# Kernel optimization log

Measured on AMD Instinct MI355X. Metric: run time of the kernel, lower is better.

Reference implementation:

```python
import jax, jax.numpy as jnp
import numpy as np

I_DECAY = 0.95
STAG_THRESH = 0.95
MAX_GATE = 0.6
MIN_I_GATE = 0.25
EPS = 1e-12


def setup_inputs() -> dict:
    key = jax.random.key(0)
    ks = jax.random.split(key, 9)
    B, T, D_IN, D_OUT = 4, 2048, 2048, 2048
    x = jax.random.normal(ks[0], (B, T, D_IN), dtype=jnp.float32)
    s = 1.0 / np.sqrt(D_IN)
    Wp = jax.random.uniform(ks[1], (D_IN, D_OUT), jnp.float32, -s, s)
    Wi = jax.random.uniform(ks[2], (D_IN, D_OUT), jnp.float32, -s, s) * 0.3
    Wd = jax.random.uniform(ks[3], (D_IN, D_OUT), jnp.float32, -s, s) * 0.3
    gate_w = jax.random.uniform(ks[4], (D_IN, 3), jnp.float32, -s, s)
    gate_b = jnp.array([0.5, 0.0, 0.0], dtype=jnp.float32)
    kick_vec = jax.random.normal(ks[5], (D_OUT,), dtype=jnp.float32) * 0.01
    kick_w = jax.random.uniform(ks[6], (D_IN, 1), jnp.float32, -s, s)
    kick_b = jnp.full((1,), -2.0, dtype=jnp.float32)
    bias = jnp.zeros((D_OUT,), dtype=jnp.float32)
    return {"x": x, "Wp": Wp, "Wi": Wi, "Wd": Wd, "gate_w": gate_w,
            "gate_b": gate_b, "kick_vec": kick_vec, "kick_w": kick_w,
            "kick_b": kick_b, "bias": bias}


def _ema_integral(x, decay):
    # x: [B,T,D] -> time-major scan; integral[0] = x[0]
    xt = jnp.swapaxes(x, 0, 1)  # [T,B,D]

    def step(carry, xcur):
        new = decay * carry + (1.0 - decay) * xcur
        return new, new

    init = xt[0]
    _, rest = jax.lax.scan(step, init, xt[1:])
    integral = jnp.concatenate([init[None], rest], axis=0)
    return jnp.swapaxes(integral, 0, 1)  # [B,T,D]


def reference(x, Wp, Wi, Wd, gate_w, gate_b, kick_vec, kick_w, kick_b, bias):
    B, T, D = x.shape
    # --- EMA integral (linear recurrence over T) ---
    integral = _ema_integral(x, I_DECAY)

    # --- stagnation-aware derivative ---
    diff = jnp.concatenate(
        [jnp.zeros_like(x[:, :1]), x[:, 1:] - x[:, :-1]], axis=1)
    x_norm = x / jnp.maximum(
        jnp.linalg.norm(x, axis=-1, keepdims=True), EPS)
    cos_sim = jnp.concatenate(
        [jnp.zeros((B, 1), x.dtype),
         jnp.sum(x_norm[:, 1:] * x_norm[:, :-1], axis=-1)], axis=1)  # [B,T]
    stagnation = (cos_sim > STAG_THRESH).astype(x.dtype)
    kick_strength = jax.nn.sigmoid(
        jnp.einsum('btd,do->bto', x, kick_w) + kick_b)[..., 0]  # [B,T]
    derivative = diff + (stagnation * kick_strength)[..., None] * kick_vec

    # --- gates: softmax -> clamp max -> clamp I min -> renormalize ---
    g = jax.nn.softmax(jnp.einsum('btd,dg->btg', x, gate_w) + gate_b, axis=-1)
    g = jnp.minimum(g, MAX_GATE)
    g = g.at[..., 1].set(jnp.maximum(g[..., 1], MIN_I_GATE))
    g = g / jnp.sum(g, axis=-1, keepdims=True)

    out = (g[..., 0:1] * jnp.einsum('btd,do->bto', x, Wp)
           + g[..., 1:2] * jnp.einsum('btd,do->bto', integral, Wi)
           + g[..., 2:3] * jnp.einsum('btd,do->bto', derivative, Wd))
    return out + bias
```

## Files before the change

### kernel.cpp

```cpp
#include <hip/hip_runtime.h>

#define DH 2048
#define TT 2048
#define BB 4
#define MROWS 8192
#define NZ 6144
#define NCH 128
#define LCH 16
#define LAM 0.44012667f
#define LAM2 1.982646e-06f

typedef __attribute__((ext_vector_type(8))) short bf16x8;
typedef __attribute__((ext_vector_type(4))) float f32x4;

__device__ __forceinline__ unsigned short f2bf(float f) {
  union { float f; unsigned int u; } v; v.f = f;
  unsigned int u = v.u;
  return (unsigned short)((u + 0x7FFFu + ((u >> 16) & 1u)) >> 16);
}
__device__ __forceinline__ float bf2f(unsigned short u) {
  union { unsigned int i; float f; } v; v.i = ((unsigned int)u) << 16;
  return v.f;
}
__device__ __forceinline__ void gld16(const unsigned short* g, unsigned short* l) {
  __builtin_amdgcn_global_load_lds((const __attribute__((address_space(1))) void*)g,
                                   (__attribute__((address_space(3))) void*)l, 16, 0, 0);
}

__global__ __launch_bounds__(256) void prep_w(const float* __restrict__ Wp,
                                              const float* __restrict__ Wi,
                                              const float* __restrict__ Wd,
                                              const float* __restrict__ kick_vec,
                                              unsigned short* __restrict__ Wt,
                                              float* __restrict__ kvWd) {
  __shared__ float tile[64][65];
  int bid = blockIdx.x;
  int mat = bid >> 10;
  int t2 = bid & 1023;
  int dt = (t2 >> 5) * 64;
  int ot = (t2 & 31) * 64;
  const float* W = (mat == 0) ? Wp : ((mat == 1) ? Wi : Wd);
  int nbase = mat * DH;
  int tid = threadIdx.x;
  int r = tid >> 4;
  int c4 = (tid & 15) * 4;
#pragma unroll
  for (int i = 0; i < 4; ++i) {
    int rr = r + i * 16;
    float4 v = *(const float4*)&W[(size_t)(dt + rr) * DH + ot + c4];
    tile[rr][c4 + 0] = v.x; tile[rr][c4 + 1] = v.y;
    tile[rr][c4 + 2] = v.z; tile[rr][c4 + 3] = v.w;
  }
  __syncthreads();
  int o = tid >> 3;
  int d8 = (tid & 7) * 8;
#pragma unroll
  for (int pass = 0; pass < 2; ++pass) {
    int oo = o + pass * 32;
    union { unsigned short u[8]; uint4 v; } pk;
#pragma unroll
    for (int i = 0; i < 8; ++i) pk.u[i] = f2bf(tile[d8 + i][oo]);
    *(uint4*)&Wt[(size_t)(nbase + ot + oo) * DH + dt + d8] = pk.v;
  }
  if (mat == 2 && tid < 64) {
    float s = 0.f;
#pragma unroll 8
    for (int dd = 0; dd < 64; ++dd) s += kick_vec[dt + dd] * tile[dd][tid];
    atomicAdd(&kvWd[ot + tid], s);
  }
}

__global__ __launch_bounds__(256) void conv_x(const float* __restrict__ x,
                                              const float* __restrict__ gate_w,
                                              const float* __restrict__ gate_b,
                                              const float* __restrict__ kick_w,
                                              const float* __restrict__ kick_b,
                                              float* __restrict__ rs,
                                              unsigned short* __restrict__ A) {
  int r = blockIdx.x;
  int t = r & (TT - 1);
  const float* xr = x + (size_t)r * DH;
  const float* xq = xr - DH;
  const bool hp = (t != 0);
  int tid = threadIdx.x;
  float a0 = 0, a1 = 0, a2 = 0, ak = 0, axx = 0, apx = 0, app = 0;
#pragma unroll
  for (int it = 0; it < 2; ++it) {
    int d0 = (tid + it * 256) * 4;
    float4 xv = *(const float4*)(xr + d0);
    float4 pv = hp ? *(const float4*)(xq + d0) : make_float4(0.f, 0.f, 0.f, 0.f);
    float4 q0 = *(const float4*)(gate_w + (size_t)d0 * 3);
    float4 q1 = *(const float4*)(gate_w + (size_t)d0 * 3 + 4);
    float4 q2 = *(const float4*)(gate_w + (size_t)d0 * 3 + 8);
    float4 kw = *(const float4*)(kick_w + d0);
    float xa[4] = {xv.x, xv.y, xv.z, xv.w};
    float pa[4] = {pv.x, pv.y, pv.z, pv.w};
    a0 += xa[0] * q0.x + xa[1] * q0.w + xa[2] * q1.z + xa[3] * q2.y;
    a1 += xa[0] * q0.y + xa[1] * q1.x + xa[2] * q1.w + xa[3] * q2.z;
    a2 += xa[0] * q0.z + xa[1] * q1.y + xa[2] * q2.x + xa[3] * q2.w;
    ak += xa[0] * kw.x + xa[1] * kw.y + xa[2] * kw.z + xa[3] * kw.w;
    union { unsigned short u[4]; uint2 v; } pk;
#pragma unroll
    for (int j = 0; j < 4; ++j) {
      axx += xa[j] * xa[j];
      apx += xa[j] * pa[j];
      app += pa[j] * pa[j];
      pk.u[j] = f2bf(xa[j]);
    }
    *(uint2*)&A[(size_t)r * DH + d0] = pk.v;
  }
#pragma unroll
  for (int off = 32; off > 0; off >>= 1) {
    a0 += __shfl_xor(a0, off); a1 += __shfl_xor(a1, off);
    a2 += __shfl_xor(a2, off); ak += __shfl_xor(ak, off);
    axx += __shfl_xor(axx, off); apx += __shfl_xor(apx, off);
    app += __shfl_xor(app, off);
  }
  __shared__ float red[4][7];
  int wv = tid >> 6;
  if ((tid & 63) == 0) {
    red[wv][0] = a0; red[wv][1] = a1; red[wv][2] = a2; red[wv][3] = ak;
    red[wv][4] = axx; red[wv][5] = apx; red[wv][6] = app;
  }
  __syncthreads();
  if (tid == 0) {
    float v[7];
#pragma unroll
    for (int i = 0; i < 7; ++i) v[i] = red[0][i] + red[1][i] + red[2][i] + red[3][i];
    float l0 = v[0] + gate_b[0], l1 = v[1] + gate_b[1], l2 = v[2] + gate_b[2];
    float mx = fmaxf(l0, fmaxf(l1, l2));
    float e0 = expf(l0 - mx), e1 = expf(l1 - mx), e2 = expf(l2 - mx);
    float inv = 1.f / (e0 + e1 + e2);
    float G0 = fminf(e0 * inv, 0.6f);
    float G1 = fminf(e1 * inv, 0.6f);
    float G2 = fminf(e2 * inv, 0.6f);
    G1 = fmaxf(G1, 0.25f);
    float inv2 = 1.f / (G0 + G1 + G2);
    G0 *= inv2; G1 *= inv2; G2 *= inv2;
    float ks = 1.f / (1.f + expf(-(v[3] + kick_b[0])));
    float nn = fmaxf(sqrtf(v[4]), 1e-12f) * fmaxf(sqrtf(v[6]), 1e-12f);
    float cs = hp ? (v[5] / nn) : 0.f;
    float cc = (cs > 0.95f) ? (G2 * ks) : 0.f;
    *(float4*)(rs + (size_t)r * 4) = make_float4(G0, G1, G2, cc);
  }
}


#define BAR __builtin_amdgcn_s_barrier()
#define VMW8 asm volatile("s_waitcnt vmcnt(8)" ::: "memory")
#define VMW4 asm volatile("s_waitcnt vmcnt(4)" ::: "memory")
#define VMW2 asm volatile("s_waitcnt vmcnt(2)" ::: "memory")
#define VMW0 asm volatile("s_waitcnt vmcnt(0)" ::: "memory")
#define LGK0 asm volatile("s_waitcnt lgkmcnt(0)" ::: "memory")

#define ST_A(bf, h, kt) do { \
  gld16(pA + (size_t)((h) * 64) * DH + (kt) * 64,       lA + (bf) * 16384 + (h) * 8192 + ldsW); \
  gld16(pA + (size_t)((h) * 64 + 128) * DH + (kt) * 64, lA + (bf) * 16384 + (h) * 8192 + 4096 + ldsW); \
} while (0)
#define ST_B(bf, g, kt) do { \
  gld16(pB + (size_t)((g) * 32) * DH + (kt) * 64,       lB + (bf) * 16384 + (g) * 8192 + ldsW); \
  gld16(pB + (size_t)((g) * 32 + 128) * DH + (kt) * 64, lB + (bf) * 16384 + (g) * 8192 + 4096 + ldsW); \
} while (0)

#define RD_A(bf, h) do { \
  const unsigned short* p_ = lA + (bf) * 16384 + (h) * 8192 + aRd; \
  _Pragma("unroll") \
  for (int mi_ = 0; mi_ < 4; ++mi_) { \
    av[mi_][0] = *(const bf16x8*)(p_ + mi_ * 1024 + kph0); \
    av[mi_][1] = *(const bf16x8*)(p_ + mi_ * 1024 + kph1); \
  } \
} while (0)
#define RD_B(bf, g) do { \
  const unsigned short* p_ = lB + (bf) * 16384 + (g) * 8192 + bRd; \
  _Pragma("unroll") \
  for (int ni_ = 0; ni_ < 2; ++ni_) { \
    bv[g][ni_][0] = *(const bf16x8*)(p_ + ni_ * 1024 + kph0); \
    bv[g][ni_][1] = *(const bf16x8*)(p_ + ni_ * 1024 + kph1); \
  } \
} while (0)

#define MM(h, g) do { \
  __builtin_amdgcn_s_setprio(1); \
  _Pragma("unroll") \
  for (int mi_ = 0; mi_ < 4; ++mi_) { \
    _Pragma("unroll") \
    for (int ni_ = 0; ni_ < 2; ++ni_) { \
      f32x4 c_ = acc[(h) * 4 + mi_][(g) * 2 + ni_]; \
      c_ = __builtin_amdgcn_mfma_f32_16x16x32_bf16(av[mi_][0], bv[g][ni_][0], c_, 0, 0, 0); \
      c_ = __builtin_amdgcn_mfma_f32_16x16x32_bf16(av[mi_][1], bv[g][ni_][1], c_, 0, 0, 0); \
      acc[(h) * 4 + mi_][(g) * 2 + ni_] = c_; \
    } \
  } \
  __builtin_amdgcn_s_setprio(0); \
} while (0)

__global__ __launch_bounds__(512, 2) void gemm_kernel(const unsigned short* __restrict__ A,
                                                      const unsigned short* __restrict__ Bt,
                                                      unsigned short* __restrict__ Z,
                                                      unsigned short* __restrict__ cpb) {
  __shared__ __align__(16) unsigned short lA[2 * 16384];
  __shared__ __align__(16) unsigned short lB[2 * 16384];
  const int tid = threadIdx.x;
  const int wave = tid >> 6, lane = tid & 63;
  const int bid = blockIdx.x;
  const int xcd = bid & 7;
  const int loc = bid >> 3;
  const int mblk = xcd * 4 + (loc & 3);
  const int nblk = loc >> 2;
  const int m0 = mblk * 256, n0 = nblk * 256;

  const int wm = wave >> 2, wn = wave & 3;
  const int rA = lane & 15, q = lane >> 4, sw = lane & 7;
  const int kph0 = ((0 + q) ^ sw) * 8;
  const int kph1 = ((4 + q) ^ sw) * 8;
  const int aRd = wm * 4096 + rA * 64;
  const int bRd = wn * 2048 + rA * 64;

  const int trow = tid >> 3;
  const int tcol = ((tid & 7) ^ (trow & 7)) * 8;
  const unsigned short* pA = A + (size_t)(m0 + trow) * DH + tcol;
  const unsigned short* pB = Bt + (size_t)(n0 + (trow >> 5) * 64 + (trow & 31)) * DH + tcol;
  const int ldsW = wave * 512;

  bf16x8 av[4][2];
  bf16x8 bv[2][2][2];
  f32x4 acc[8][4] = {};

  ST_A(0, 0, 0); ST_B(0, 0, 0); ST_B(0, 1, 0); ST_A(0, 1, 0);
  ST_A(1, 0, 1); ST_B(1, 0, 1);
  VMW8; BAR;

#pragma unroll 1
  for (int i = 0; i < 15; ++i) {
    const int t1 = 2 * i + 1, t2 = 2 * i + 2, t3 = 2 * i + 3;
    RD_A(0, 0); RD_B(0, 0); ST_B(1, 1, t1); VMW8; BAR; LGK0; MM(0, 0); BAR;
    RD_B(0, 1);             ST_A(1, 1, t1); VMW8; BAR; LGK0; MM(0, 1); BAR;
    RD_A(0, 1);             ST_A(0, 0, t2);       BAR; LGK0; MM(1, 0); BAR;
                            ST_B(0, 0, t2); VMW8; BAR; LGK0; MM(1, 1); BAR;
    RD_A(1, 0); RD_B(1, 0); ST_B(0, 1, t2); VMW8; BAR; LGK0; MM(0, 0); BAR;
    RD_B(1, 1);             ST_A(0, 1, t2); VMW8; BAR; LGK0; MM(0, 1); BAR;
    RD_A(1, 1);             ST_A(1, 0, t3);       BAR; LGK0; MM(1, 0); BAR;
                            ST_B(1, 0, t3); VMW8; BAR; LGK0; MM(1, 1); BAR;
  }
  RD_A(0, 0); RD_B(0, 0); ST_B(1, 1, 31); VMW8; BAR; LGK0; MM(0, 0); BAR;
  RD_B(0, 1);             ST_A(1, 1, 31); VMW8; BAR; LGK0; MM(0, 1); BAR;
  RD_A(0, 1);                                   BAR; LGK0; MM(1, 0); BAR;
                                          VMW4; BAR; LGK0; MM(1, 1); BAR;
  RD_A(1, 0); RD_B(1, 0);                 VMW2; BAR; LGK0; MM(0, 0); BAR;
  RD_B(1, 1);                             VMW0; BAR; LGK0; MM(0, 1); BAR;
  RD_A(1, 1);                                   BAR; LGK0; MM(1, 0); BAR;
                                                            MM(1, 1);

  const int mbase = m0 + wm * 128;
  const int nbase = n0 + wn * 64;

  if (nblk >= 8 && nblk < 16) {
    float w12 = (q == 3) ? 1.0f : (q == 2) ? 0.81450625f
              : (q == 1) ? 0.66342043f : 0.54036009f;
    w12 *= 0.05f;
#pragma unroll
    for (int mi = 0; mi < 8; ++mi) {
      const int mrow = mbase + mi * 16;
      const int bb = mrow >> 11;
      const int chh = (mrow >> 4) & (NCH - 1);
      const bool first = (chh == 0);
#pragma unroll
      for (int ni = 0; ni < 4; ++ni) {
        float v0 = acc[mi][ni][0];
        float s = ((v0 * 0.95f + acc[mi][ni][1]) * 0.95f + acc[mi][ni][2]) * 0.95f
                  + acc[mi][ni][3];
        if (first && q == 0) s += 19.0f * 0.857375f * v0;
        s *= w12;
        s += __shfl_xor(s, 16);
        s += __shfl_xor(s, 32);
        if (q == 0) {
          int nloc = nbase + ni * 16 + rA - 2048;
          cpb[((size_t)bb * NCH + chh) * DH + nloc] = f2bf(s);
        }
      }
    }
  }

#pragma unroll
  for (int ni = 0; ni < 4; ++ni) {
    const int n = nbase + ni * 16 + rA;
#pragma unroll
    for (int mi = 0; mi < 8; ++mi) {
#pragma unroll
      for (int rg = 0; rg < 4; ++rg) {
        const int m = mbase + mi * 16 + q * 4 + rg;
        Z[(size_t)m * NZ + n] = f2bf(acc[mi][ni][rg]);
      }
    }
  }
}

#undef BAR
#undef VMW8
#undef VMW4
#undef VMW2
#undef VMW0
#undef LGK0
#undef ST_A
#undef ST_B
#undef RD_A
#undef RD_B
#undef MM

__global__ __launch_bounds__(256) void zi_p1(unsigned short* __restrict__ cpb,
                                             float* __restrict__ gc) {
  int gid = blockIdx.x * 256 + threadIdx.x;
  int n = gid & (DH - 1);
  int g = (gid >> 11) & 7;
  int b = gid >> 14;
  float run = 0.f;
#pragma unroll
  for (int j = 0; j < 16; ++j) {
    size_t idx = ((size_t)b * NCH + g * 16 + j) * DH + n;
    float c = bf2f(cpb[idx]);
    cpb[idx] = f2bf(run);
    run = c + LAM * run;
  }
  gc[((size_t)b * 8 + g) * DH + n] = run;
}

__global__ __launch_bounds__(256) void zi_p2(float* __restrict__ gc) {
  int gid = blockIdx.x * 256 + threadIdx.x;
  int n = gid & (DH - 1);
  int b = gid >> 11;
  float run = 0.f;
#pragma unroll
  for (int g = 0; g < 8; ++g) {
    size_t idx = ((size_t)b * 8 + g) * DH + n;
    float old = gc[idx];
    gc[idx] = run;
    run = old + LAM2 * run;
  }
}

__global__ __launch_bounds__(256) void final_combine(const unsigned short* __restrict__ Z,
                                                     const float* __restrict__ rs,
                                                     const unsigned short* __restrict__ cpb,
                                                     const float* __restrict__ gc,
                                                     const float* __restrict__ kvWd,
                                                     const float* __restrict__ bias,
                                                     float* __restrict__ out) {
  int tid = threadIdx.x;
  int n = blockIdx.y * 1024 + tid * 4;
  int ch = blockIdx.x & (NCH - 1);
  int b = blockIdx.x >> 7;
  int r0 = b * TT + ch * LCH;
  const unsigned short* zb = Z + (size_t)r0 * NZ + n;
  const bool first_chunk = (ch == 0);

  int g = ch >> 4, j = ch & 15;
  float pw = 1.f;
  for (int i = 0; i < j; ++i) pw *= LAM;
  float Pv[4];
  {
    union { unsigned short u[4]; uint2 v; } c;
    c.v = *(const uint2*)&cpb[((size_t)b * NCH + ch) * DH + n];
    float4 gp = *(const float4*)&gc[((size_t)b * 8 + g) * DH + n];
    float gpa[4] = {gp.x, gp.y, gp.z, gp.w};
#pragma unroll
    for (int i = 0; i < 4; ++i) Pv[i] = bf2f(c.u[i]) + pw * gpa[i];
  }
  float kv[4], bz[4];
  {
    float4 k0 = *(const float4*)&kvWd[n];
    float4 b0 = *(const float4*)&bias[n];
    kv[0]=k0.x; kv[1]=k0.y; kv[2]=k0.z; kv[3]=k0.w;
    bz[0]=b0.x; bz[1]=b0.y; bz[2]=b0.z; bz[3]=b0.w;
  }
  float zdp[4];
  if (!first_chunk) {
    union { unsigned short u[4]; uint2 v; } c;
    c.v = *(const uint2*)(zb - NZ + 2 * DH);
#pragma unroll
    for (int i = 0; i < 4; ++i) zdp[i] = bf2f(c.u[i]);
  } else {
#pragma unroll
    for (int i = 0; i < 4; ++i) zdp[i] = 0.f;
  }
  float J[4];
#pragma unroll
  for (int i = 0; i < 4; ++i) J[i] = 0.f;
  float f = 1.f;
  uint2 cp = *(const uint2*)(zb);
  uint2 ci = *(const uint2*)(zb + DH);
  uint2 cd = *(const uint2*)(zb + 2 * DH);
#pragma unroll
  for (int tau = 0; tau < LCH; ++tau) {
    uint2 np, ni, nd;
    if (tau < LCH - 1) {
      const unsigned short* zn = zb + (size_t)(tau + 1) * NZ;
      np = *(const uint2*)(zn);
      ni = *(const uint2*)(zn + DH);
      nd = *(const uint2*)(zn + 2 * DH);
    }
    float4 gg = *(const float4*)&rs[(size_t)(r0 + tau) * 4];
    union { unsigned short u[4]; uint2 v; } up, ui, ud;
    up.v = cp; ui.v = ci; ud.v = cd;
    const bool vfirst = first_chunk && (tau == 0);
    f *= 0.95f;
    float o[4];
#pragma unroll
    for (int i = 0; i < 4; ++i) {
      float xp = bf2f(up.u[i]), xi = bf2f(ui.u[i]), xd = bf2f(ud.u[i]);
      if (vfirst) J[i] = xi;
      else J[i] = 0.95f * J[i] + 0.05f * xi;
      float I = J[i] + f * Pv[i];
      float diff = vfirst ? 0.f : (xd - zdp[i]);
      o[i] = gg.x * xp + gg.y * I + gg.z * diff + gg.w * kv[i] + bz[i];
      zdp[i] = xd;
    }
    *(float4*)(out + (size_t)(r0 + tau) * DH + n) = make_float4(o[0], o[1], o[2], o[3]);
    cp = np; ci = ni; cd = nd;
  }
}

extern "C" void kernel_launch(void* const* d_in, const int* in_sizes, int n_in,
                              void* d_out, int out_size, void* d_ws, size_t ws_size,
                              hipStream_t stream) {
  const float* x        = (const float*)d_in[0];
  const float* Wp       = (const float*)d_in[1];
  const float* Wi       = (const float*)d_in[2];
  const float* Wd       = (const float*)d_in[3];
  const float* gate_w   = (const float*)d_in[4];
  const float* gate_b   = (const float*)d_in[5];
  const float* kick_vec = (const float*)d_in[6];
  const float* kick_w   = (const float*)d_in[7];
  const float* kick_b   = (const float*)d_in[8];
  const float* bias     = (const float*)d_in[9];
  float* out = (float*)d_out;

  char* ws = (char*)d_ws;
  unsigned short* Wt  = (unsigned short*)(ws + 0);
  unsigned short* Z   = (unsigned short*)(ws + 25165824);
  float* rs   = (float*)(ws + 125829120);
  float* kvWd = (float*)(ws + 125960192);
  unsigned short* cpb = (unsigned short*)(ws + 125968384);
  float* gc   = (float*)(ws + 128065536);
  unsigned short* A = (unsigned short*)d_out;
  (void)ws_size; (void)in_sizes; (void)n_in; (void)out_size;

  hipMemsetAsync(kvWd, 0, DH * sizeof(float), stream);
  prep_w<<<dim3(3072), dim3(256), 0, stream>>>(Wp, Wi, Wd, kick_vec, Wt, kvWd);
  conv_x<<<dim3(8192), dim3(256), 0, stream>>>(x, gate_w, gate_b, kick_w, kick_b, rs, A);
  gemm_kernel<<<dim3(768), dim3(512), 0, stream>>>(A, Wt, Z, cpb);
  zi_p1<<<dim3(256), dim3(256), 0, stream>>>(cpb, gc);
  zi_p2<<<dim3(32), dim3(256), 0, stream>>>(gc);
  final_combine<<<dim3(512, 2), dim3(256), 0, stream>>>(Z, rs, cpb, gc, kvWd, bias, out);
}
```

Before: 419.0 us.

## Reschedule GEMM global-to-LDS prefetch to wait once per half-iteration

Reorders the staged global-to-LDS loads in the main GEMM loop so one extra B tile is prefetched in the prologue. Each half-iteration now has a single vmcnt(6) wait instead of several vmcnt(8) waits, and an lgkmcnt(8) wait is added after the LDS reads. The goal is fewer memory stalls and barriers blocking on loads, giving more overlap of loads with MFMA work. The epilogue store loop is also reordered to iterate n innermost, which may change write coalescing. Getting the wait counts wrong could cause races, so correctness depends on exact counter accounting.

```diff
diff --git a/kernel.cpp b/kernel.cpp
--- a/kernel.cpp
+++ b/kernel.cpp
@@ -147,10 +147,9 @@
 
 
 #define BAR __builtin_amdgcn_s_barrier()
-#define VMW8 asm volatile("s_waitcnt vmcnt(8)" ::: "memory")
-#define VMW4 asm volatile("s_waitcnt vmcnt(4)" ::: "memory")
-#define VMW2 asm volatile("s_waitcnt vmcnt(2)" ::: "memory")
+#define VMW6 asm volatile("s_waitcnt vmcnt(6)" ::: "memory")
 #define VMW0 asm volatile("s_waitcnt vmcnt(0)" ::: "memory")
+#define LGK8 asm volatile("s_waitcnt lgkmcnt(8)" ::: "memory")
 #define LGK0 asm volatile("s_waitcnt lgkmcnt(0)" ::: "memory")
 
 #define ST_A(bf, h, kt) do { \
@@ -227,29 +226,29 @@
   f32x4 acc[8][4] = {};
 
   ST_A(0, 0, 0); ST_B(0, 0, 0); ST_B(0, 1, 0); ST_A(0, 1, 0);
-  ST_A(1, 0, 1); ST_B(1, 0, 1);
-  VMW8; BAR;
+  ST_A(1, 0, 1); ST_B(1, 0, 1); ST_B(1, 1, 1);
+  VMW6; BAR;
 
 #pragma unroll 1
   for (int i = 0; i < 15; ++i) {
     const int t1 = 2 * i + 1, t2 = 2 * i + 2, t3 = 2 * i + 3;
-    RD_A(0, 0); RD_B(0, 0); ST_B(1, 1, t1); VMW8; BAR; LGK0; MM(0, 0); BAR;
-    RD_B(0, 1);             ST_A(1, 1, t1); VMW8; BAR; LGK0; MM(0, 1); BAR;
-    RD_A(0, 1);             ST_A(0, 0, t2);       BAR; LGK0; MM(1, 0); BAR;
-                            ST_B(0, 0, t2); VMW8; BAR; LGK0; MM(1, 1); BAR;
-    RD_A(1, 0); RD_B(1, 0); ST_B(0, 1, t2); VMW8; BAR; LGK0; MM(0, 0); BAR;
-    RD_B(1, 1);             ST_A(0, 1, t2); VMW8; BAR; LGK0; MM(0, 1); BAR;
-    RD_A(1, 1);             ST_A(1, 0, t3);       BAR; LGK0; MM(1, 0); BAR;
-                            ST_B(1, 0, t3); VMW8; BAR; LGK0; MM(1, 1); BAR;
-  }
-  RD_A(0, 0); RD_B(0, 0); ST_B(1, 1, 31); VMW8; BAR; LGK0; MM(0, 0); BAR;
-  RD_B(0, 1);             ST_A(1, 1, 31); VMW8; BAR; LGK0; MM(0, 1); BAR;
+    RD_A(0, 0); RD_B(0, 0); ST_A(1, 1, t1); LGK8; BAR; LGK0; MM(0, 0); BAR;
+    RD_B(0, 1);             ST_A(0, 0, t2);       BAR; LGK0; MM(0, 1); BAR;
+    RD_A(0, 1);             ST_B(0, 0, t2);       BAR; LGK0; MM(1, 0); BAR;
+                            ST_B(0, 1, t2); VMW6; BAR;       MM(1, 1); BAR;
+    RD_A(1, 0); RD_B(1, 0); ST_A(0, 1, t2); LGK8; BAR; LGK0; MM(0, 0); BAR;
+    RD_B(1, 1);             ST_A(1, 0, t3);       BAR; LGK0; MM(0, 1); BAR;
+    RD_A(1, 1);             ST_B(1, 0, t3);       BAR; LGK0; MM(1, 0); BAR;
+                            ST_B(1, 1, t3); VMW6; BAR;       MM(1, 1); BAR;
+  }
+  RD_A(0, 0); RD_B(0, 0); ST_A(1, 1, 31); LGK8; BAR; LGK0; MM(0, 0); BAR;
+  RD_B(0, 1);                                   BAR; LGK0; MM(0, 1); BAR;
   RD_A(0, 1);                                   BAR; LGK0; MM(1, 0); BAR;
-                                          VMW4; BAR; LGK0; MM(1, 1); BAR;
-  RD_A(1, 0); RD_B(1, 0);                 VMW2; BAR; LGK0; MM(0, 0); BAR;
-  RD_B(1, 1);                             VMW0; BAR; LGK0; MM(0, 1); BAR;
+                                          VMW0; BAR;       MM(1, 1); BAR;
+  RD_A(1, 0); RD_B(1, 0);                       BAR; LGK0; MM(0, 0); BAR;
+  RD_B(1, 1);                                   BAR; LGK0; MM(0, 1); BAR;
   RD_A(1, 1);                                   BAR; LGK0; MM(1, 0); BAR;
-                                                            MM(1, 1);
+                                                           MM(1, 1);
 
   const int mbase = m0 + wm * 128;
   const int nbase = n0 + wn * 64;
@@ -282,13 +281,13 @@
   }
 
 #pragma unroll
-  for (int ni = 0; ni < 4; ++ni) {
-    const int n = nbase + ni * 16 + rA;
-#pragma unroll
-    for (int mi = 0; mi < 8; ++mi) {
-#pragma unroll
-      for (int rg = 0; rg < 4; ++rg) {
-        const int m = mbase + mi * 16 + q * 4 + rg;
+  for (int mi = 0; mi < 8; ++mi) {
+#pragma unroll
+    for (int rg = 0; rg < 4; ++rg) {
+      const int m = mbase + mi * 16 + q * 4 + rg;
+#pragma unroll
+      for (int ni = 0; ni < 4; ++ni) {
+        const int n = nbase + ni * 16 + rA;
         Z[(size_t)m * NZ + n] = f2bf(acc[mi][ni][rg]);
       }
     }
@@ -296,10 +295,9 @@
 }
 
 #undef BAR
-#undef VMW8
-#undef VMW4
-#undef VMW2
+#undef VMW6
 #undef VMW0
+#undef LGK8
 #undef LGK0
 #undef ST_A
 #undef ST_B
```

Result: faster. 390.2 us (-6.9%).
